# Performance work log

Hardware: AMD Instinct MI355X
Metric: run time of the kernel (lower is better)

The kernel has to match this reference:

```python
import jax, jax.numpy as jnp
import numpy as np

N_NODES = 50000
N_EDGES = 1000000
N_GRAPHS = 64
IN_FEATS, HIDDEN, N_CLASSES = 64, 64, 32


def setup_inputs() -> dict:
    key = jax.random.key(0)
    ks = jax.random.split(key, 10)
    x = jax.random.normal(ks[0], (N_NODES, IN_FEATS), dtype=jnp.float32)
    eh = jax.random.normal(ks[1], (N_EDGES,), dtype=jnp.float32)
    src = jax.random.randint(ks[2], (N_EDGES,), 0, N_NODES)
    dst = jax.random.randint(ks[3], (N_EDGES,), 0, N_NODES)
    node_graph = jnp.sort(jax.random.randint(ks[4], (N_NODES,), 0, N_GRAPHS))
    # GraphConv parameters (glorot-ish scale)
    W1 = jax.random.normal(ks[5], (IN_FEATS, HIDDEN), dtype=jnp.float32) / np.sqrt(IN_FEATS)
    b1 = jnp.zeros((HIDDEN,), dtype=jnp.float32)
    W2 = jax.random.normal(ks[6], (HIDDEN, N_CLASSES), dtype=jnp.float32) / np.sqrt(HIDDEN)
    b2 = jnp.zeros((N_CLASSES,), dtype=jnp.float32)
    mu = jnp.array(0.0, dtype=jnp.float32)
    # sigma = -1.0 keeps log((eh-mu)^2 / -sigma) in a valid domain (module default 1.0 -> NaN)
    sigma = jnp.array(-1.0, dtype=jnp.float32)
    return {"x": x, "eh": eh, "src": src, "dst": dst, "node_graph": node_graph,
            "W1": W1, "b1": b1, "W2": W2, "b2": b2, "mu": mu, "sigma": sigma}


def _graph_conv(x, W, b, src, dst, ew, norm_src, norm_dst):
    # DGL GraphConv(norm='both') with per-edge scalar weight ew:
    # h = D_in^{-1/2} * A_w * (D_out^{-1/2} * x) @ W + b
    xs = x * norm_src  # [N, F]
    msg = xs[src] * ew[:, None]  # gather + edge-weight multiply  [E, F]
    agg = jax.ops.segment_sum(msg, dst, num_segments=x.shape[0])  # scatter-add [N, F]
    return (agg * norm_dst) @ W + b


def reference(x, eh, src, dst, node_graph, W1, b1, W2, b2, mu, sigma):
    n = x.shape[0]
    ones_e = jnp.ones_like(eh)
    deg_out = jnp.clip(jax.ops.segment_sum(ones_e, src, num_segments=n), 1.0)
    deg_in = jnp.clip(jax.ops.segment_sum(ones_e, dst, num_segments=n), 1.0)
    norm_src = jax.lax.rsqrt(deg_out)[:, None]  # [N,1]
    norm_dst = jax.lax.rsqrt(deg_in)[:, None]   # [N,1]

    # edge feature transform: log((h - mu)^2 / -sigma)
    d = eh - mu
    efeat = jnp.log(d * d / -sigma)  # [E]

    h = _graph_conv(x, W1, b1, src, dst, efeat, norm_src, norm_dst)
    h = jax.nn.relu(h)
    h = _graph_conv(h, W2, b2, src, dst, efeat, norm_src, norm_dst)

    # dgl.mean_nodes: per-graph mean over nodes
    g_sum = jax.ops.segment_sum(h, node_graph, num_segments=N_GRAPHS)  # [B, C]
    g_cnt = jnp.clip(jax.ops.segment_sum(jnp.ones((n,), jnp.float32), node_graph,
                                         num_segments=N_GRAPHS), 1.0)
    return g_sum / g_cnt[:, None]
```

## Files before the change

kernel.cpp:

```cpp
#include <hip/hip_runtime.h>

#define NGRAPHS 64
#define NCLS 32
#define G1 256

__device__ inline unsigned bfpack(float lo, float hi) {
    unsigned ulo = __float_as_uint(lo); ulo += 0x7fffu + ((ulo >> 16) & 1u);
    unsigned uhi = __float_as_uint(hi); uhi += 0x7fffu + ((uhi >> 16) & 1u);
    return (ulo >> 16) | (uhi & 0xffff0000u);
}
__device__ inline float bflo(unsigned p) { return __uint_as_float(p << 16); }
__device__ inline float bfhi(unsigned p) { return __uint_as_float(p & 0xffff0000u); }
__device__ inline float bfs(unsigned short u) { return __uint_as_float((unsigned)u << 16); }

__global__ __launch_bounds__(256) void part_hist(const int* __restrict__ src,
    const int* __restrict__ dst, int* __restrict__ gHd, int* __restrict__ gHs,
    int* __restrict__ gLocD, int* __restrict__ gLocS, int nE) {
    __shared__ int hd[256], hs[256], tmp[256];
    int t = threadIdx.x, blk = blockIdx.x;
    hd[t] = 0; hs[t] = 0;
    __syncthreads();
    int chunk = (nE + G1 - 1) / G1;
    int beg = blk * chunk, end = min(beg + chunk, nE);
    for (int i = beg + t; i < end; i += 256) {
        atomicAdd(&hd[((unsigned)dst[i]) >> 8], 1);
        atomicAdd(&hs[((unsigned)src[i]) >> 8], 1);
    }
    __syncthreads();
    gHd[t * G1 + blk] = hd[t];
    gHs[t * G1 + blk] = hs[t];
    tmp[t] = hd[t];
    __syncthreads();
    for (int o = 1; o < 256; o <<= 1) {
        int u = (t >= o) ? tmp[t - o] : 0;
        __syncthreads();
        tmp[t] += u;
        __syncthreads();
    }
    gLocD[blk * 256 + t] = tmp[t] - hd[t];
    __syncthreads();
    tmp[t] = hs[t];
    __syncthreads();
    for (int o = 1; o < 256; o <<= 1) {
        int u = (t >= o) ? tmp[t - o] : 0;
        __syncthreads();
        tmp[t] += u;
        __syncthreads();
    }
    gLocS[blk * 256 + t] = tmp[t] - hs[t];
}

__global__ __launch_bounds__(1024) void part_scan(int* __restrict__ a, int* __restrict__ b) {
    __shared__ int part[1024];
    int* arr = blockIdx.x ? b : a;
    int t = threadIdx.x;
    int base = t * 64;
    int v[64], s = 0;
#pragma unroll
    for (int j = 0; j < 64; ++j) { v[j] = arr[base + j]; s += v[j]; }
    part[t] = s;
    __syncthreads();
    for (int o = 1; o < 1024; o <<= 1) {
        int u = (t >= o) ? part[t - o] : 0;
        __syncthreads();
        part[t] += u;
        __syncthreads();
    }
    int run = part[t] - s;
#pragma unroll
    for (int j = 0; j < 64; ++j) { arr[base + j] = run; run += v[j]; }
    if (t == 1023) arr[65536] = run;
}

__global__ __launch_bounds__(256) void part_scatter(const float* __restrict__ eh,
    const int* __restrict__ src, const int* __restrict__ dst,
    const float* __restrict__ mu, const float* __restrict__ sigma,
    const int* __restrict__ gLocD, const int* __restrict__ gLocS,
    int2* __restrict__ partD, unsigned char* __restrict__ partS, int nE) {
    __shared__ int hd[256], hs[256], locD[256], locS[256];
    int t = threadIdx.x, blk = blockIdx.x;
    hd[t] = 0; hs[t] = 0;
    locD[t] = gLocD[blk * 256 + t];
    locS[t] = gLocS[blk * 256 + t];
    __syncthreads();
    float mu0 = mu[0], inv = -1.f / sigma[0];
    int chunk = (nE + G1 - 1) / G1;
    size_t wbase = (size_t)blk * chunk;
    int beg = blk * chunk, end = min(beg + chunk, nE);
    for (int i = beg + t; i < end; i += 256) {
        int d = dst[i], s = src[i];
        float df = eh[i] - mu0;
        float w = logf(df * df * inv);
        int bu = ((unsigned)d) >> 8;
        int r = atomicAdd(&hd[bu], 1);
        partD[wbase + locD[bu] + r] = make_int2((s << 8) | (d & 255), __float_as_int(w));
        int bs = ((unsigned)s) >> 8;
        int r2 = atomicAdd(&hs[bs], 1);
        partS[wbase + locS[bs] + r2] = (unsigned char)(s & 255);
    }
}

__global__ __launch_bounds__(256) void bucket_build(const int2* __restrict__ partD,
    const unsigned char* __restrict__ partS, const int* __restrict__ gHd,
    const int* __restrict__ gHs, const int* __restrict__ gLocD,
    const int* __restrict__ gLocS, int* __restrict__ csr_src,
    unsigned short* __restrict__ csr_w, int* __restrict__ row_start,
    float* __restrict__ norm_dst, float* __restrict__ norm_src, int nN, int nE) {
    __shared__ int deg[256], loff[256], cnt[256];
    int b = blockIdx.x, t = threadIdx.x;
    int chunk = (nE + G1 - 1) / G1;
    int begD = gHd[b * G1];
    int lenD = gHd[b * G1 + t + 1] - gHd[b * G1 + t];
    size_t offD = (size_t)t * chunk + gLocD[t * 256 + b];
    deg[t] = 0; cnt[t] = 0;
    __syncthreads();
    for (int i = 0; i < lenD; ++i)
        atomicAdd(&deg[partD[offD + i].x & 255], 1);
    __syncthreads();
    loff[t] = deg[t];
    __syncthreads();
    for (int o = 1; o < 256; o <<= 1) {
        int u = (t >= o) ? loff[t - o] : 0;
        __syncthreads();
        loff[t] += u;
        __syncthreads();
    }
    loff[t] -= deg[t];
    __syncthreads();
    int n = b * 256 + t;
    if (n < nN) {
        row_start[n] = begD + loff[t];
        norm_dst[n] = rsqrtf((float)max(deg[t], 1));
    }
    if (b == 0 && t == 0) row_start[nN] = nE;
    for (int i = 0; i < lenD; ++i) {
        int2 r = partD[offD + i];
        int lo = r.x & 255;
        int pos = atomicAdd(&cnt[lo], 1);
        int idx = begD + loff[lo] + pos;
        csr_src[idx] = r.x >> 8;
        unsigned uw = (unsigned)r.y;
        csr_w[idx] = (unsigned short)((uw + 0x7fffu + ((uw >> 16) & 1u)) >> 16);
    }
    __syncthreads();
    deg[t] = 0;
    __syncthreads();
    int lenS = gHs[b * G1 + t + 1] - gHs[b * G1 + t];
    size_t offS = (size_t)t * chunk + gLocS[t * 256 + b];
    for (int i = 0; i < lenS; ++i)
        atomicAdd(&deg[partS[offS + i]], 1);
    __syncthreads();
    if (n < nN) norm_src[n] = rsqrtf((float)max(deg[t], 1));
}

__global__ __launch_bounds__(256) void xw_mm(const float* __restrict__ x,
    const float* __restrict__ norm_src, const float* __restrict__ W1,
    unsigned* __restrict__ xw, int nN) {
    __shared__ float sW[64 * 64];
    __shared__ float srow[4][64];
    int t = threadIdx.x;
    for (int i = t; i < 64 * 64; i += 256) sW[i] = W1[i];
    __syncthreads();
    int wid = t >> 6, k = t & 63;
    int base = blockIdx.x * 32;
    for (int it = 0; it < 8; ++it) {
        int n = base + it * 4 + wid;
        if (n >= nN) break;
        srow[wid][k] = x[((size_t)n << 6) + k] * norm_src[n];
        float acc0 = 0.f, acc1 = 0.f;
#pragma unroll
        for (int i = 0; i < 64; i += 2) {
            acc0 += srow[wid][i] * sW[i * 64 + k];
            acc1 += srow[wid][i + 1] * sW[(i + 1) * 64 + k];
        }
        float outv = acc0 + acc1;
        float other = __shfl_xor(outv, 1, 64);
        if ((k & 1) == 0) xw[((size_t)n << 5) + (k >> 1)] = bfpack(outv, other);
    }
}

#define LCSR(P, bg, en) { \
    int last_ = max((en) - 1, 0); \
    _Pragma("unroll") \
    for (int u = 0; u < 6; ++u) { \
        int sl = (bg) + q + 4 * u; \
        int slc = (sl < (en)) ? sl : last_; \
        P##s[u] = csr_src[slc]; \
        float wv = bfs(csr_w[slc]); \
        P##w[u] = (sl < (en)) ? wv : 0.f; \
    } }
#define LGAT(P) { \
    _Pragma("unroll") \
    for (int u = 0; u < 6; ++u) P##p[u] = xw2[((size_t)P##s[u] << 4) + j]; }
#define LFMA(P) { \
    _Pragma("unroll") \
    for (int u = 0; u < 6; ++u) { \
        a0 += P##w[u] * bflo(P##p[u].x); a1 += P##w[u] * bfhi(P##p[u].x); \
        a2 += P##w[u] * bflo(P##p[u].y); a3 += P##w[u] * bfhi(P##p[u].y); } }
#define REM(P, bg, en) { \
    for (int sl0 = (bg) + q + 24; sl0 < (en); sl0 += 24) { \
        int last_ = (en) - 1; \
        _Pragma("unroll") \
        for (int u = 0; u < 6; ++u) { \
            int sl = sl0 + 4 * u; \
            int slc = (sl < (en)) ? sl : last_; \
            P##s[u] = csr_src[slc]; \
            float wv = bfs(csr_w[slc]); \
            P##w[u] = (sl < (en)) ? wv : 0.f; } \
        _Pragma("unroll") \
        for (int u = 0; u < 6; ++u) P##p[u] = xw2[((size_t)P##s[u] << 4) + j]; \
        LFMA(P) } }
#define EPI(nd_, ns_, n_) { \
    a0 += __shfl_xor(a0, 16, 64); a0 += __shfl_xor(a0, 32, 64); \
    a1 += __shfl_xor(a1, 16, 64); a1 += __shfl_xor(a1, 32, 64); \
    a2 += __shfl_xor(a2, 16, 64); a2 += __shfl_xor(a2, 32, 64); \
    a3 += __shfl_xor(a3, 16, 64); a3 += __shfl_xor(a3, 32, 64); \
    if (q == 0) { \
        float4 v; \
        v.x = fmaxf(a0 * (nd_) + bv.x, 0.f) * (ns_); \
        v.y = fmaxf(a1 * (nd_) + bv.y, 0.f) * (ns_); \
        v.z = fmaxf(a2 * (nd_) + bv.z, 0.f) * (ns_); \
        v.w = fmaxf(a3 * (nd_) + bv.w, 0.f) * (ns_); \
        *reinterpret_cast<float4*>(&srow[wid][4 * j]) = v; } \
    { int jj = lane & 31, ib = lane & 32; \
      float c0 = 0.f, c1 = 0.f; \
      _Pragma("unroll") \
      for (int i = 0; i < 32; i += 2) { \
          c0 += srow[wid][ib + i] * sW[(ib + i) * NCLS + jj]; \
          c1 += srow[wid][ib + i + 1] * sW[(ib + i + 1) * NCLS + jj]; } \
      float part = c0 + c1; \
      part += __shfl_xor(part, 32, 64); \
      float other = __shfl_xor(part, 1, 64); \
      if (ib == 0 && (jj & 1) == 0 && (n_) < nN) \
          hw[((size_t)(n_) << 4) + (jj >> 1)] = bfpack(part, other); } }

__global__ __launch_bounds__(256) void gather1_mm(const unsigned* __restrict__ xw,
    const int* __restrict__ row_start, const int* __restrict__ csr_src,
    const unsigned short* __restrict__ csr_w, const float* __restrict__ norm_dst,
    const float* __restrict__ norm_src, const float* __restrict__ W2f,
    const float* __restrict__ b1, unsigned* __restrict__ hw, int nN) {
    __shared__ float sW[64 * NCLS];
    __shared__ float srow[4][64];
    __shared__ int rs[17];
    int t = threadIdx.x;
    int base = blockIdx.x * 16;
    for (int i = t; i < 64 * NCLS; i += 256) sW[i] = W2f[i];
    if (t < 17) rs[t] = row_start[min(base + t, nN)];
    __syncthreads();
    int wid = t >> 6, lane = t & 63;
    int q = lane >> 4, j = lane & 15;
    const uint2* xw2 = reinterpret_cast<const uint2*>(xw);
    float4 bv = reinterpret_cast<const float4*>(b1)[j];
    int n0 = base + wid, n1 = n0 + 4, n2 = n0 + 8, n3 = n0 + 12;
    int nc = nN - 1;
    float nd0 = norm_dst[min(n0, nc)], ns0 = norm_src[min(n0, nc)];
    float nd1 = norm_dst[min(n1, nc)], ns1 = norm_src[min(n1, nc)];
    float nd2 = norm_dst[min(n2, nc)], ns2 = norm_src[min(n2, nc)];
    float nd3 = norm_dst[min(n3, nc)], ns3 = norm_src[min(n3, nc)];
    int r0b = __builtin_amdgcn_readfirstlane(rs[wid]);
    int r0e = __builtin_amdgcn_readfirstlane(rs[wid + 1]);
    int r1b = __builtin_amdgcn_readfirstlane(rs[wid + 4]);
    int r1e = __builtin_amdgcn_readfirstlane(rs[wid + 5]);
    int r2b = __builtin_amdgcn_readfirstlane(rs[wid + 8]);
    int r2e = __builtin_amdgcn_readfirstlane(rs[wid + 9]);
    int r3b = __builtin_amdgcn_readfirstlane(rs[wid + 12]);
    int r3e = __builtin_amdgcn_readfirstlane(rs[wid + 13]);
    int As[6]; float Aw[6]; uint2 Ap[6];
    int Bs[6]; float Bw[6]; uint2 Bp[6];
    float a0, a1, a2, a3;
    LCSR(A, r0b, r0e)
    LGAT(A)
    LCSR(B, r1b, r1e)
    LGAT(B)
    a0 = a1 = a2 = a3 = 0.f;
    LFMA(A)
    REM(A, r0b, r0e)
    LCSR(A, r2b, r2e)
    EPI(nd0, ns0, n0)
    LGAT(A)
    a0 = a1 = a2 = a3 = 0.f;
    LFMA(B)
    REM(B, r1b, r1e)
    LCSR(B, r3b, r3e)
    EPI(nd1, ns1, n1)
    LGAT(B)
    a0 = a1 = a2 = a3 = 0.f;
    LFMA(A)
    REM(A, r2b, r2e)
    EPI(nd2, ns2, n2)
    a0 = a1 = a2 = a3 = 0.f;
    LFMA(B)
    REM(B, r3b, r3e)
    EPI(nd3, ns3, n3)
}

#define LCSR2(P, bg, en) { \
    int last_ = max((en) - 1, 0); \
    _Pragma("unroll") \
    for (int u = 0; u < 2; ++u) { \
        int sl = (bg) + o + 8 * u; \
        int slc = (sl < (en)) ? sl : last_; \
        P##s[u] = csr_src[slc]; \
        float wv = bfs(csr_w[slc]); \
        P##w[u] = (sl < (en)) ? wv : 0.f; \
    } }
#define LGAT2(P) { \
    _Pragma("unroll") \
    for (int u = 0; u < 2; ++u) P##p[u] = hw2[((size_t)P##s[u] << 3) + j]; }
#define LFMA2(P) { \
    _Pragma("unroll") \
    for (int u = 0; u < 2; ++u) { \
        a0 += P##w[u] * bflo(P##p[u].x); a1 += P##w[u] * bfhi(P##p[u].x); \
        a2 += P##w[u] * bflo(P##p[u].y); a3 += P##w[u] * bfhi(P##p[u].y); } }
#define REM2(P, bg, en) { \
    for (int sl0 = (bg) + o + 16; sl0 < (en); sl0 += 16) { \
        int last_ = (en) - 1; \
        _Pragma("unroll") \
        for (int u = 0; u < 2; ++u) { \
            int sl = sl0 + 8 * u; \
            int slc = (sl < (en)) ? sl : last_; \
            P##s[u] = csr_src[slc]; \
            float wv = bfs(csr_w[slc]); \
            P##w[u] = (sl < (en)) ? wv : 0.f; } \
        _Pragma("unroll") \
        for (int u = 0; u < 2; ++u) P##p[u] = hw2[((size_t)P##s[u] << 3) + j]; \
        LFMA2(P) } }
#define EPI2(nd_, n_) { \
    a0 += __shfl_xor(a0, 8, 64); a0 += __shfl_xor(a0, 16, 64); a0 += __shfl_xor(a0, 32, 64); \
    a1 += __shfl_xor(a1, 8, 64); a1 += __shfl_xor(a1, 16, 64); a1 += __shfl_xor(a1, 32, 64); \
    a2 += __shfl_xor(a2, 8, 64); a2 += __shfl_xor(a2, 16, 64); a2 += __shfl_xor(a2, 32, 64); \
    a3 += __shfl_xor(a3, 8, 64); a3 += __shfl_xor(a3, 16, 64); a3 += __shfl_xor(a3, 32, 64); \
    if (lane < 8 && (n_) < nN) { \
        uint2 outv; \
        outv.x = bfpack(a0 * (nd_), a1 * (nd_)); \
        outv.y = bfpack(a2 * (nd_), a3 * (nd_)); \
        reinterpret_cast<uint2*>(agg2)[((size_t)(n_) << 3) + j] = outv; } }

__global__ __launch_bounds__(256) void gather2(const unsigned* __restrict__ hw,
    const int* __restrict__ row_start, const int* __restrict__ csr_src,
    const unsigned short* __restrict__ csr_w, const float* __restrict__ norm_dst,
    unsigned* __restrict__ agg2, int nN) {
    __shared__ int rs[17];
    int t = threadIdx.x;
    int base = blockIdx.x * 16;
    if (t < 17) rs[t] = row_start[min(base + t, nN)];
    __syncthreads();
    int wid = t >> 6, lane = t & 63;
    int o = lane >> 3, j = lane & 7;
    const uint2* hw2 = reinterpret_cast<const uint2*>(hw);
    int n0 = base + wid, n1 = n0 + 4, n2 = n0 + 8, n3 = n0 + 12;
    int nc = nN - 1;
    float nd0 = norm_dst[min(n0, nc)], nd1 = norm_dst[min(n1, nc)];
    float nd2 = norm_dst[min(n2, nc)], nd3 = norm_dst[min(n3, nc)];
    int r0b = __builtin_amdgcn_readfirstlane(rs[wid]);
    int r0e = __builtin_amdgcn_readfirstlane(rs[wid + 1]);
    int r1b = __builtin_amdgcn_readfirstlane(rs[wid + 4]);
    int r1e = __builtin_amdgcn_readfirstlane(rs[wid + 5]);
    int r2b = __builtin_amdgcn_readfirstlane(rs[wid + 8]);
    int r2e = __builtin_amdgcn_readfirstlane(rs[wid + 9]);
    int r3b = __builtin_amdgcn_readfirstlane(rs[wid + 12]);
    int r3e = __builtin_amdgcn_readfirstlane(rs[wid + 13]);
    int As[2]; float Aw[2]; uint2 Ap[2];
    int Bs[2]; float Bw[2]; uint2 Bp[2];
    float a0, a1, a2, a3;
    LCSR2(A, r0b, r0e)
    LGAT2(A)
    LCSR2(B, r1b, r1e)
    LGAT2(B)
    a0 = a1 = a2 = a3 = 0.f;
    LFMA2(A)
    REM2(A, r0b, r0e)
    LCSR2(A, r2b, r2e)
    EPI2(nd0, n0)
    LGAT2(A)
    a0 = a1 = a2 = a3 = 0.f;
    LFMA2(B)
    REM2(B, r1b, r1e)
    LCSR2(B, r3b, r3e)
    EPI2(nd1, n1)
    LGAT2(B)
    a0 = a1 = a2 = a3 = 0.f;
    LFMA2(A)
    REM2(A, r2b, r2e)
    EPI2(nd2, n2)
    a0 = a1 = a2 = a3 = 0.f;
    LFMA2(B)
    REM2(B, r3b, r3e)
    EPI2(nd3, n3)
}

__global__ __launch_bounds__(256) void pool_out(const unsigned* __restrict__ agg2,
    const int* __restrict__ ng, const float* __restrict__ b2,
    float* __restrict__ out, int nN) {
    __shared__ float gacc[NCLS];
    int g = blockIdx.x, t = threadIdx.x;
    if (t < NCLS) gacc[t] = 0.f;
    __syncthreads();
    int lo = 0, hi = nN;
    while (lo < hi) { int m = (lo + hi) >> 1; if (ng[m] < g) lo = m + 1; else hi = m; }
    int lb = lo;
    lo = 0; hi = nN;
    while (lo < hi) { int m = (lo + hi) >> 1; if (ng[m] < g + 1) lo = m + 1; else hi = m; }
    int ub = lo;
    int r = t >> 4, j = t & 15;
    float ax = 0.f, ay = 0.f;
    for (int n = lb + r; n < ub; n += 16) {
        unsigned p = agg2[((size_t)n << 4) + j];
        ax += bflo(p); ay += bfhi(p);
    }
    atomicAdd(&gacc[2 * j], ax);
    atomicAdd(&gacc[2 * j + 1], ay);
    __syncthreads();
    if (t < NCLS) {
        float cnt = (float)(ub - lb);
        out[g * NCLS + t] = (gacc[t] + b2[t] * cnt) / fmaxf(cnt, 1.f);
    }
}

extern "C" void kernel_launch(void* const* d_in, const int* in_sizes, int n_in,
                              void* d_out, int out_size, void* d_ws, size_t ws_size,
                              hipStream_t stream) {
    const float* x   = (const float*)d_in[0];
    const float* eh  = (const float*)d_in[1];
    const int*   src = (const int*)d_in[2];
    const int*   dst = (const int*)d_in[3];
    const int*   ng  = (const int*)d_in[4];
    const float* W1  = (const float*)d_in[5];
    const float* b1  = (const float*)d_in[6];
    const float* W2  = (const float*)d_in[7];
    const float* b2  = (const float*)d_in[8];
    const float* mu  = (const float*)d_in[9];
    const float* sg  = (const float*)d_in[10];
    const int nN = in_sizes[0] / 64;
    const int nE = in_sizes[1];
    const int NBUK = (nN + 255) / 256;
    const int chunk = (nE + G1 - 1) / G1;

    char* wsb = (char*)d_ws;
    int* gHd = (int*)wsb;
    int* gHs = gHd + 65537;
    int* gLocD = gHs + 65537;
    int* gLocS = gLocD + 65536;
    int* row_start = gLocS + 65536;
    float* norm_src = (float*)(row_start + nN + 1);
    float* norm_dst = norm_src + nN;
    size_t off = (size_t)((char*)(norm_dst + nN) - wsb);
    off = (off + 15) & ~(size_t)15;
    int2* partD = (int2*)(wsb + off);
    unsigned char* partS = (unsigned char*)(partD + (size_t)G1 * chunk);
    off = (size_t)((char*)(partS + (size_t)G1 * chunk) - wsb);
    off = (off + 15) & ~(size_t)15;
    int* csr_src = (int*)(wsb + off);
    unsigned short* csr_w = (unsigned short*)(csr_src + nE);
    off = (size_t)((char*)(csr_w + nE) - wsb);
    off = (off + 15) & ~(size_t)15;
    unsigned* xw   = (unsigned*)(wsb + off);
    unsigned* hw   = xw + (size_t)nN * 32;
    unsigned* agg2 = hw + (size_t)nN * 16;

    part_hist<<<G1, 256, 0, stream>>>(src, dst, gHd, gHs, gLocD, gLocS, nE);
    part_scan<<<2, 1024, 0, stream>>>(gHd, gHs);
    part_scatter<<<G1, 256, 0, stream>>>(eh, src, dst, mu, sg, gLocD, gLocS,
                                         partD, partS, nE);
    bucket_build<<<NBUK, 256, 0, stream>>>(partD, partS, gHd, gHs, gLocD, gLocS,
                                           csr_src, csr_w, row_start,
                                           norm_dst, norm_src, nN, nE);
    xw_mm<<<(nN + 31) / 32, 256, 0, stream>>>(x, norm_src, W1, xw, nN);
    gather1_mm<<<(nN + 15) / 16, 256, 0, stream>>>(xw, row_start, csr_src, csr_w,
                                                   norm_dst, norm_src, W2, b1, hw, nN);
    gather2<<<(nN + 15) / 16, 256, 0, stream>>>(hw, row_start, csr_src, csr_w,
                                                norm_dst, agg2, nN);
    pool_out<<<NGRAPHS, 256, 0, stream>>>(agg2, ng, b2, (float*)d_out, nN);

    (void)n_in; (void)out_size; (void)ws_size;
}
```

Before: 169.6 us.

## Replace partitioned bucket CSR build with global atomic histogram and cursor scatter

Replaces the two-level partition/bucket sort CSR construction with a direct approach: zero per-node degree arrays, count in- and out-degrees with global atomics, scan once in a single block that also writes normalisation factors, then scatter edges via atomic per-row cursors. This removes the intermediate partition buffers and the serial per-bucket loops. In exchange it relies on many global atomics and uncoalesced random writes, and the edge order within each row becomes nondeterministic.

After: 422.7 us. 149% more time.

```diff
diff --git a/kernel.cpp b/kernel.cpp
--- a/kernel.cpp
+++ b/kernel.cpp
@@ -2,7 +2,6 @@
 
 #define NGRAPHS 64
 #define NCLS 32
-#define G1 256
 
 __device__ inline unsigned bfpack(float lo, float hi) {
     unsigned ulo = __float_as_uint(lo); ulo += 0x7fffu + ((ulo >> 16) & 1u);
@@ -13,51 +12,37 @@
 __device__ inline float bfhi(unsigned p) { return __uint_as_float(p & 0xffff0000u); }
 __device__ inline float bfs(unsigned short u) { return __uint_as_float((unsigned)u << 16); }
 
-__global__ __launch_bounds__(256) void part_hist(const int* __restrict__ src,
-    const int* __restrict__ dst, int* __restrict__ gHd, int* __restrict__ gHs,
-    int* __restrict__ gLocD, int* __restrict__ gLocS, int nE) {
-    __shared__ int hd[256], hs[256], tmp[256];
-    int t = threadIdx.x, blk = blockIdx.x;
-    hd[t] = 0; hs[t] = 0;
-    __syncthreads();
-    int chunk = (nE + G1 - 1) / G1;
-    int beg = blk * chunk, end = min(beg + chunk, nE);
-    for (int i = beg + t; i < end; i += 256) {
-        atomicAdd(&hd[((unsigned)dst[i]) >> 8], 1);
-        atomicAdd(&hs[((unsigned)src[i]) >> 8], 1);
-    }
-    __syncthreads();
-    gHd[t * G1 + blk] = hd[t];
-    gHs[t * G1 + blk] = hs[t];
-    tmp[t] = hd[t];
-    __syncthreads();
-    for (int o = 1; o < 256; o <<= 1) {
-        int u = (t >= o) ? tmp[t - o] : 0;
-        __syncthreads();
-        tmp[t] += u;
-        __syncthreads();
-    }
-    gLocD[blk * 256 + t] = tmp[t] - hd[t];
-    __syncthreads();
-    tmp[t] = hs[t];
-    __syncthreads();
-    for (int o = 1; o < 256; o <<= 1) {
-        int u = (t >= o) ? tmp[t - o] : 0;
-        __syncthreads();
-        tmp[t] += u;
-        __syncthreads();
-    }
-    gLocS[blk * 256 + t] = tmp[t] - hs[t];
-}
-
-__global__ __launch_bounds__(1024) void part_scan(int* __restrict__ a, int* __restrict__ b) {
+__global__ __launch_bounds__(256) void zero2(int* __restrict__ degD,
+    int* __restrict__ degS, int nN) {
+    int i = blockIdx.x * 256 + threadIdx.x;
+    if (i < nN) { degD[i] = 0; degS[i] = 0; }
+}
+
+__global__ __launch_bounds__(256) void deg_hist(const int* __restrict__ src,
+    const int* __restrict__ dst, int* __restrict__ degD, int* __restrict__ degS,
+    int nE) {
+    int i = blockIdx.x * 256 + threadIdx.x;
+    int stride = gridDim.x * 256;
+    for (; i < nE; i += stride) {
+        atomicAdd(&degD[dst[i]], 1);
+        atomicAdd(&degS[src[i]], 1);
+    }
+}
+
+__global__ __launch_bounds__(1024) void scan_norm(const int* __restrict__ degD,
+    const int* __restrict__ degS, int* __restrict__ row_start,
+    int* __restrict__ cursor, float* __restrict__ norm_dst,
+    float* __restrict__ norm_src, int nN, int nE) {
     __shared__ int part[1024];
-    int* arr = blockIdx.x ? b : a;
     int t = threadIdx.x;
     int base = t * 64;
     int v[64], s = 0;
 #pragma unroll
-    for (int j = 0; j < 64; ++j) { v[j] = arr[base + j]; s += v[j]; }
+    for (int j = 0; j < 64; ++j) {
+        int idx = base + j;
+        v[j] = (idx < nN) ? degD[idx] : 0;
+        s += v[j];
+    }
     part[t] = s;
     __syncthreads();
     for (int o = 1; o < 1024; o <<= 1) {
@@ -68,89 +53,36 @@
     }
     int run = part[t] - s;
 #pragma unroll
-    for (int j = 0; j < 64; ++j) { arr[base + j] = run; run += v[j]; }
-    if (t == 1023) arr[65536] = run;
-}
-
-__global__ __launch_bounds__(256) void part_scatter(const float* __restrict__ eh,
+    for (int j = 0; j < 64; ++j) {
+        int idx = base + j;
+        if (idx < nN) {
+            row_start[idx] = run;
+            cursor[idx] = run;
+            norm_dst[idx] = rsqrtf((float)max(v[j], 1));
+            norm_src[idx] = rsqrtf((float)max(degS[idx], 1));
+        }
+        run += v[j];
+    }
+    if (t == 1023) row_start[nN] = nE;
+}
+
+__global__ __launch_bounds__(256) void scatter_csr(const float* __restrict__ eh,
     const int* __restrict__ src, const int* __restrict__ dst,
     const float* __restrict__ mu, const float* __restrict__ sigma,
-    const int* __restrict__ gLocD, const int* __restrict__ gLocS,
-    int2* __restrict__ partD, unsigned char* __restrict__ partS, int nE) {
-    __shared__ int hd[256], hs[256], locD[256], locS[256];
-    int t = threadIdx.x, blk = blockIdx.x;
-    hd[t] = 0; hs[t] = 0;
-    locD[t] = gLocD[blk * 256 + t];
-    locS[t] = gLocS[blk * 256 + t];
-    __syncthreads();
+    int* __restrict__ cursor, int* __restrict__ csr_src,
+    unsigned short* __restrict__ csr_w, int nE) {
     float mu0 = mu[0], inv = -1.f / sigma[0];
-    int chunk = (nE + G1 - 1) / G1;
-    size_t wbase = (size_t)blk * chunk;
-    int beg = blk * chunk, end = min(beg + chunk, nE);
-    for (int i = beg + t; i < end; i += 256) {
+    int i = blockIdx.x * 256 + threadIdx.x;
+    int stride = gridDim.x * 256;
+    for (; i < nE; i += stride) {
         int d = dst[i], s = src[i];
         float df = eh[i] - mu0;
         float w = logf(df * df * inv);
-        int bu = ((unsigned)d) >> 8;
-        int r = atomicAdd(&hd[bu], 1);
-        partD[wbase + locD[bu] + r] = make_int2((s << 8) | (d & 255), __float_as_int(w));
-        int bs = ((unsigned)s) >> 8;
-        int r2 = atomicAdd(&hs[bs], 1);
-        partS[wbase + locS[bs] + r2] = (unsigned char)(s & 255);
-    }
-}
-
-__global__ __launch_bounds__(256) void bucket_build(const int2* __restrict__ partD,
-    const unsigned char* __restrict__ partS, const int* __restrict__ gHd,
-    const int* __restrict__ gHs, const int* __restrict__ gLocD,
-    const int* __restrict__ gLocS, int* __restrict__ csr_src,
-    unsigned short* __restrict__ csr_w, int* __restrict__ row_start,
-    float* __restrict__ norm_dst, float* __restrict__ norm_src, int nN, int nE) {
-    __shared__ int deg[256], loff[256], cnt[256];
-    int b = blockIdx.x, t = threadIdx.x;
-    int chunk = (nE + G1 - 1) / G1;
-    int begD = gHd[b * G1];
-    int lenD = gHd[b * G1 + t + 1] - gHd[b * G1 + t];
-    size_t offD = (size_t)t * chunk + gLocD[t * 256 + b];
-    deg[t] = 0; cnt[t] = 0;
-    __syncthreads();
-    for (int i = 0; i < lenD; ++i)
-        atomicAdd(&deg[partD[offD + i].x & 255], 1);
-    __syncthreads();
-    loff[t] = deg[t];
-    __syncthreads();
-    for (int o = 1; o < 256; o <<= 1) {
-        int u = (t >= o) ? loff[t - o] : 0;
-        __syncthreads();
-        loff[t] += u;
-        __syncthreads();
-    }
-    loff[t] -= deg[t];
-    __syncthreads();
-    int n = b * 256 + t;
-    if (n < nN) {
-        row_start[n] = begD + loff[t];
-        norm_dst[n] = rsqrtf((float)max(deg[t], 1));
-    }
-    if (b == 0 && t == 0) row_start[nN] = nE;
-    for (int i = 0; i < lenD; ++i) {
-        int2 r = partD[offD + i];
-        int lo = r.x & 255;
-        int pos = atomicAdd(&cnt[lo], 1);
-        int idx = begD + loff[lo] + pos;
-        csr_src[idx] = r.x >> 8;
-        unsigned uw = (unsigned)r.y;
-        csr_w[idx] = (unsigned short)((uw + 0x7fffu + ((uw >> 16) & 1u)) >> 16);
-    }
-    __syncthreads();
-    deg[t] = 0;
-    __syncthreads();
-    int lenS = gHs[b * G1 + t + 1] - gHs[b * G1 + t];
-    size_t offS = (size_t)t * chunk + gLocS[t * 256 + b];
-    for (int i = 0; i < lenS; ++i)
-        atomicAdd(&deg[partS[offS + i]], 1);
-    __syncthreads();
-    if (n < nN) norm_src[n] = rsqrtf((float)max(deg[t], 1));
+        int pos = atomicAdd(&cursor[d], 1);
+        csr_src[pos] = s;
+        unsigned uw = __float_as_uint(w);
+        csr_w[pos] = (unsigned short)((uw + 0x7fffu + ((uw >> 16) & 1u)) >> 16);
+    }
 }
 
 __global__ __launch_bounds__(256) void xw_mm(const float* __restrict__ x,
@@ -433,22 +365,15 @@
     const float* sg  = (const float*)d_in[10];
     const int nN = in_sizes[0] / 64;
     const int nE = in_sizes[1];
-    const int NBUK = (nN + 255) / 256;
-    const int chunk = (nE + G1 - 1) / G1;
 
     char* wsb = (char*)d_ws;
-    int* gHd = (int*)wsb;
-    int* gHs = gHd + 65537;
-    int* gLocD = gHs + 65537;
-    int* gLocS = gLocD + 65536;
-    int* row_start = gLocS + 65536;
-    float* norm_src = (float*)(row_start + nN + 1);
+    int* degD = (int*)wsb;
+    int* degS = degD + nN;
+    int* row_start = degS + nN;
+    int* cursor = row_start + nN + 1;
+    float* norm_src = (float*)(cursor + nN);
     float* norm_dst = norm_src + nN;
     size_t off = (size_t)((char*)(norm_dst + nN) - wsb);
-    off = (off + 15) & ~(size_t)15;
-    int2* partD = (int2*)(wsb + off);
-    unsigned char* partS = (unsigned char*)(partD + (size_t)G1 * chunk);
-    off = (size_t)((char*)(partS + (size_t)G1 * chunk) - wsb);
     off = (off + 15) & ~(size_t)15;
     int* csr_src = (int*)(wsb + off);
     unsigned short* csr_w = (unsigned short*)(csr_src + nE);
@@ -458,13 +383,12 @@
     unsigned* hw   = xw + (size_t)nN * 32;
     unsigned* agg2 = hw + (size_t)nN * 16;
 
-    part_hist<<<G1, 256, 0, stream>>>(src, dst, gHd, gHs, gLocD, gLocS, nE);
-    part_scan<<<2, 1024, 0, stream>>>(gHd, gHs);
-    part_scatter<<<G1, 256, 0, stream>>>(eh, src, dst, mu, sg, gLocD, gLocS,
-                                         partD, partS, nE);
-    bucket_build<<<NBUK, 256, 0, stream>>>(partD, partS, gHd, gHs, gLocD, gLocS,
-                                           csr_src, csr_w, row_start,
-                                           norm_dst, norm_src, nN, nE);
+    zero2<<<(nN + 255) / 256, 256, 0, stream>>>(degD, degS, nN);
+    deg_hist<<<2048, 256, 0, stream>>>(src, dst, degD, degS, nE);
+    scan_norm<<<1, 1024, 0, stream>>>(degD, degS, row_start, cursor,
+                                      norm_dst, norm_src, nN, nE);
+    scatter_csr<<<2048, 256, 0, stream>>>(eh, src, dst, mu, sg, cursor,
+                                          csr_src, csr_w, nE);
     xw_mm<<<(nN + 31) / 32, 256, 0, stream>>>(x, norm_src, W1, xw, nN);
     gather1_mm<<<(nN + 15) / 16, 256, 0, stream>>>(xw, row_start, csr_src, csr_w,
                                                    norm_dst, norm_src, W2, b1, hw, nN);
```

## Fuse partition histogram and scatter into one kernel; batch loads in bucket build

Applied to the files above, without the earlier changes.

The per-block histogram and the scatter into partitioned buffers now run in one kernel. The local bucket offsets stay in shared memory, and the scatter no longer waits for the global scan, because it only needs block-local offsets relative to the block's chunk base. This removes a kernel launch and a second read of src/dst/gLocD. Separately, the bucket_build loops load four or eight partition entries ahead before doing the shared atomics, to raise memory-level parallelism on the serial per-thread loops.

Result: faster. 165.4 us (-2.5%).

```diff
diff --git a/kernel.cpp b/kernel.cpp
--- a/kernel.cpp
+++ b/kernel.cpp
@@ -13,10 +13,13 @@
 __device__ inline float bfhi(unsigned p) { return __uint_as_float(p & 0xffff0000u); }
 __device__ inline float bfs(unsigned short u) { return __uint_as_float((unsigned)u << 16); }
 
-__global__ __launch_bounds__(256) void part_hist(const int* __restrict__ src,
-    const int* __restrict__ dst, int* __restrict__ gHd, int* __restrict__ gHs,
-    int* __restrict__ gLocD, int* __restrict__ gLocS, int nE) {
-    __shared__ int hd[256], hs[256], tmp[256];
+__global__ __launch_bounds__(256) void part_hist_scatter(
+    const float* __restrict__ eh, const int* __restrict__ src,
+    const int* __restrict__ dst, const float* __restrict__ mu,
+    const float* __restrict__ sigma, int* __restrict__ gHd,
+    int* __restrict__ gHs, int* __restrict__ gLocD, int* __restrict__ gLocS,
+    int2* __restrict__ partD, unsigned char* __restrict__ partS, int nE) {
+    __shared__ int hd[256], hs[256], tmp[256], locD[256], locS[256];
     int t = threadIdx.x, blk = blockIdx.x;
     hd[t] = 0; hs[t] = 0;
     __syncthreads();
@@ -37,7 +40,8 @@
         tmp[t] += u;
         __syncthreads();
     }
-    gLocD[blk * 256 + t] = tmp[t] - hd[t];
+    locD[t] = tmp[t] - hd[t];
+    gLocD[blk * 256 + t] = locD[t];
     __syncthreads();
     tmp[t] = hs[t];
     __syncthreads();
@@ -47,46 +51,12 @@
         tmp[t] += u;
         __syncthreads();
     }
-    gLocS[blk * 256 + t] = tmp[t] - hs[t];
-}
-
-__global__ __launch_bounds__(1024) void part_scan(int* __restrict__ a, int* __restrict__ b) {
-    __shared__ int part[1024];
-    int* arr = blockIdx.x ? b : a;
-    int t = threadIdx.x;
-    int base = t * 64;
-    int v[64], s = 0;
-#pragma unroll
-    for (int j = 0; j < 64; ++j) { v[j] = arr[base + j]; s += v[j]; }
-    part[t] = s;
-    __syncthreads();
-    for (int o = 1; o < 1024; o <<= 1) {
-        int u = (t >= o) ? part[t - o] : 0;
-        __syncthreads();
-        part[t] += u;
-        __syncthreads();
-    }
-    int run = part[t] - s;
-#pragma unroll
-    for (int j = 0; j < 64; ++j) { arr[base + j] = run; run += v[j]; }
-    if (t == 1023) arr[65536] = run;
-}
-
-__global__ __launch_bounds__(256) void part_scatter(const float* __restrict__ eh,
-    const int* __restrict__ src, const int* __restrict__ dst,
-    const float* __restrict__ mu, const float* __restrict__ sigma,
-    const int* __restrict__ gLocD, const int* __restrict__ gLocS,
-    int2* __restrict__ partD, unsigned char* __restrict__ partS, int nE) {
-    __shared__ int hd[256], hs[256], locD[256], locS[256];
-    int t = threadIdx.x, blk = blockIdx.x;
+    locS[t] = tmp[t] - hs[t];
+    gLocS[blk * 256 + t] = locS[t];
     hd[t] = 0; hs[t] = 0;
-    locD[t] = gLocD[blk * 256 + t];
-    locS[t] = gLocS[blk * 256 + t];
     __syncthreads();
     float mu0 = mu[0], inv = -1.f / sigma[0];
-    int chunk = (nE + G1 - 1) / G1;
     size_t wbase = (size_t)blk * chunk;
-    int beg = blk * chunk, end = min(beg + chunk, nE);
     for (int i = beg + t; i < end; i += 256) {
         int d = dst[i], s = src[i];
         float df = eh[i] - mu0;
@@ -98,6 +68,28 @@
         int r2 = atomicAdd(&hs[bs], 1);
         partS[wbase + locS[bs] + r2] = (unsigned char)(s & 255);
     }
+}
+
+__global__ __launch_bounds__(1024) void part_scan(int* __restrict__ a, int* __restrict__ b) {
+    __shared__ int part[1024];
+    int* arr = blockIdx.x ? b : a;
+    int t = threadIdx.x;
+    int base = t * 64;
+    int v[64], s = 0;
+#pragma unroll
+    for (int j = 0; j < 64; ++j) { v[j] = arr[base + j]; s += v[j]; }
+    part[t] = s;
+    __syncthreads();
+    for (int o = 1; o < 1024; o <<= 1) {
+        int u = (t >= o) ? part[t - o] : 0;
+        __syncthreads();
+        part[t] += u;
+        __syncthreads();
+    }
+    int run = part[t] - s;
+#pragma unroll
+    for (int j = 0; j < 64; ++j) { arr[base + j] = run; run += v[j]; }
+    if (t == 1023) arr[65536] = run;
 }
 
 __global__ __launch_bounds__(256) void bucket_build(const int2* __restrict__ partD,
@@ -114,8 +106,15 @@
     size_t offD = (size_t)t * chunk + gLocD[t * 256 + b];
     deg[t] = 0; cnt[t] = 0;
     __syncthreads();
-    for (int i = 0; i < lenD; ++i)
-        atomicAdd(&deg[partD[offD + i].x & 255], 1);
+    for (int i = 0; i < lenD; i += 4) {
+        int lo4[4];
+#pragma unroll
+        for (int u = 0; u < 4; ++u)
+            lo4[u] = partD[offD + min(i + u, lenD - 1)].x & 255;
+#pragma unroll
+        for (int u = 0; u < 4; ++u)
+            if (i + u < lenD) atomicAdd(&deg[lo4[u]], 1);
+    }
     __syncthreads();
     loff[t] = deg[t];
     __syncthreads();
@@ -133,22 +132,37 @@
         norm_dst[n] = rsqrtf((float)max(deg[t], 1));
     }
     if (b == 0 && t == 0) row_start[nN] = nE;
-    for (int i = 0; i < lenD; ++i) {
-        int2 r = partD[offD + i];
-        int lo = r.x & 255;
-        int pos = atomicAdd(&cnt[lo], 1);
-        int idx = begD + loff[lo] + pos;
-        csr_src[idx] = r.x >> 8;
-        unsigned uw = (unsigned)r.y;
-        csr_w[idx] = (unsigned short)((uw + 0x7fffu + ((uw >> 16) & 1u)) >> 16);
+    for (int i = 0; i < lenD; i += 4) {
+        int2 r4[4];
+#pragma unroll
+        for (int u = 0; u < 4; ++u)
+            r4[u] = partD[offD + min(i + u, lenD - 1)];
+#pragma unroll
+        for (int u = 0; u < 4; ++u) {
+            if (i + u < lenD) {
+                int lo = r4[u].x & 255;
+                int pos = atomicAdd(&cnt[lo], 1);
+                int idx = begD + loff[lo] + pos;
+                csr_src[idx] = r4[u].x >> 8;
+                unsigned uw = (unsigned)r4[u].y;
+                csr_w[idx] = (unsigned short)((uw + 0x7fffu + ((uw >> 16) & 1u)) >> 16);
+            }
+        }
     }
     __syncthreads();
     deg[t] = 0;
     __syncthreads();
     int lenS = gHs[b * G1 + t + 1] - gHs[b * G1 + t];
     size_t offS = (size_t)t * chunk + gLocS[t * 256 + b];
-    for (int i = 0; i < lenS; ++i)
-        atomicAdd(&deg[partS[offS + i]], 1);
+    for (int i = 0; i < lenS; i += 8) {
+        int v8[8];
+#pragma unroll
+        for (int u = 0; u < 8; ++u)
+            v8[u] = partS[offS + min(i + u, lenS - 1)];
+#pragma unroll
+        for (int u = 0; u < 8; ++u)
+            if (i + u < lenS) atomicAdd(&deg[v8[u]], 1);
+    }
     __syncthreads();
     if (n < nN) norm_src[n] = rsqrtf((float)max(deg[t], 1));
 }
@@ -458,10 +472,9 @@
     unsigned* hw   = xw + (size_t)nN * 32;
     unsigned* agg2 = hw + (size_t)nN * 16;
 
-    part_hist<<<G1, 256, 0, stream>>>(src, dst, gHd, gHs, gLocD, gLocS, nE);
+    part_hist_scatter<<<G1, 256, 0, stream>>>(eh, src, dst, mu, sg, gHd, gHs,
+                                              gLocD, gLocS, partD, partS, nE);
     part_scan<<<2, 1024, 0, stream>>>(gHd, gHs);
-    part_scatter<<<G1, 256, 0, stream>>>(eh, src, dst, mu, sg, gLocD, gLocS,
-                                         partD, partS, nE);
     bucket_build<<<NBUK, 256, 0, stream>>>(partD, partS, gHd, gHs, gLocD, gLocS,
                                            csr_src, csr_w, row_start,
                                            norm_dst, norm_src, nN, nE);
```
